# Kernel tuning notes

Hardware: AMD Instinct MI355X
Metric: run time of the kernel (lower is better)

## Reference

```python
import jax, jax.numpy as jnp
import numpy as np

N_HEADS = 16


def setup_inputs() -> dict:
    key = jax.random.key(0)
    ks = jax.random.split(key, 6)
    B, S, E = 2, 2048, 1024
    scale = 1.0 / np.sqrt(E)
    return {
        "X": jax.random.normal(ks[0], (B, S, E), dtype=jnp.float32),
        "Wq": jax.random.normal(ks[1], (E, E), dtype=jnp.float32) * scale,
        "Wk": jax.random.normal(ks[2], (E, E), dtype=jnp.float32) * scale,
        "Wv": jax.random.normal(ks[3], (E, E), dtype=jnp.float32) * scale,
        "Wp": jax.random.normal(ks[4], (E, E), dtype=jnp.float32) * scale,
        "bp": jnp.zeros((E,), dtype=jnp.float32),
    }


def reference(X, Wq, Wk, Wv, Wp, bp):
    B, S, E = X.shape
    H = N_HEADS
    dk = E // H
    # qkv projections (Linear with weight [out,in] -> x @ W.T), split heads
    q = (X @ Wq.T).reshape(B, S, H, dk).transpose(0, 2, 1, 3)  # [B,H,S,dk]
    k = (X @ Wk.T).reshape(B, S, H, dk).transpose(0, 2, 1, 3)
    v = (X @ Wv.T).reshape(B, S, H, dk).transpose(0, 2, 1, 3)
    scores = jnp.einsum('bhqd,bhkd->bhqk', q, k) / jnp.sqrt(jnp.asarray(dk, X.dtype))
    causal = jnp.tril(jnp.ones((S, S), dtype=bool))  # [S,S]
    scores = jnp.where(causal[None, None], scores, jnp.asarray(-jnp.inf, X.dtype))
    attn = jax.nn.softmax(scores, axis=-1)  # [B,H,S,S]
    y = jnp.einsum('bhqk,bhkd->bhqd', attn, v)  # [B,H,S,dk]
    y = y.transpose(0, 2, 1, 3).reshape(B, S, E)
    return y @ Wp.T + bp
```

## Files before the change

### kernel.cpp

```cpp
#include <hip/hip_runtime.h>

typedef unsigned short u16;
typedef __bf16 bf16x8 __attribute__((ext_vector_type(8)));
typedef float f32x4 __attribute__((ext_vector_type(4)));
typedef unsigned short u16x8 __attribute__((ext_vector_type(8)));
typedef unsigned short u16x4 __attribute__((ext_vector_type(4)));

union B8 { u16x8 u; bf16x8 b; };

#define MFMA_BF16(a, b, c) __builtin_amdgcn_mfma_f32_16x16x32_bf16((a), (b), (c), 0, 0, 0)

__device__ __forceinline__ u16 f2bf(float f) {
  unsigned x = __float_as_uint(f);
  unsigned r = x + 0x7fffu + ((x >> 16) & 1u);
  return (u16)(r >> 16);
}

__device__ __forceinline__ unsigned cvt_pk_bf16(float lo, float hi) {
  unsigned r;
  asm("v_cvt_pk_bf16_f32 %0, %1, %2" : "=v"(r) : "v"(lo), "v"(hi));
  return r;
}

__device__ __forceinline__ void gl2lds16(const void* g, void* l) {
  __builtin_amdgcn_global_load_lds(
      (const __attribute__((address_space(1))) void*)g,
      (__attribute__((address_space(3))) void*)l, 16, 0, 0);
}

__global__ __launch_bounds__(256) void cast5_kernel(
    const float* __restrict__ X, const float* __restrict__ Wq,
    const float* __restrict__ Wk, const float* __restrict__ Wv,
    const float* __restrict__ Wp, u16* __restrict__ Xb, u16* __restrict__ Wqb,
    u16* __restrict__ Wkb, u16* __restrict__ Wvb, u16* __restrict__ Wpb) {
  size_t i = ((size_t)blockIdx.x * 256 + threadIdx.x) * 4;
  const float* src;
  u16* dst;
  size_t off;
  if (i < 4194304) {
    src = X; dst = Xb; off = i;
  } else if (i < 5242880) {
    src = Wq; dst = Wqb; off = i - 4194304;
  } else if (i < 6291456) {
    src = Wk; dst = Wkb; off = i - 5242880;
  } else if (i < 7340032) {
    src = Wv; dst = Wvb; off = i - 6291456;
  } else {
    src = Wp; dst = Wpb; off = i - 7340032;
  }
  float4 v = *(const float4*)(src + off);
  u16x4 o;
  o[0] = f2bf(v.x); o[1] = f2bf(v.y); o[2] = f2bf(v.z); o[3] = f2bf(v.w);
  *(u16x4*)(dst + off) = o;
}

template <int N0>
__device__ __forceinline__ void mfma16(f32x4 (&acc)[8][4], B8 (&af)[8], B8& b0,
                                       B8& b1) {
  __builtin_amdgcn_s_setprio(1);
#pragma unroll
  for (int m = 0; m < 8; ++m) {
    acc[m][N0] = MFMA_BF16(af[m].b, b0.b, acc[m][N0]);
    acc[m][N0 + 1] = MFMA_BF16(af[m].b, b1.b, acc[m][N0 + 1]);
  }
  __builtin_amdgcn_s_setprio(0);
}

__global__ __launch_bounds__(512, 2) void gemm_qkv256(
    const u16* __restrict__ Xb, const u16* __restrict__ Wb,
    u16* __restrict__ Qb, u16* __restrict__ Kb, u16* __restrict__ Vt) {
  __shared__ __align__(16) u16 Al[2][2][256 * 32];
  __shared__ __align__(16) u16 Bl[2][2][256 * 32];

  int tid = threadIdx.x, lane = tid & 63, w = tid >> 6;
  int wr = w >> 2, wc = w & 3;
  int l16 = lane & 15, lg = lane >> 4;

  int bid = blockIdx.x;
  int swz = (bid & 7) * 24 + (bid >> 3);
  int bm = swz / 12, bn = swz % 12;

  const u16* Ag = Xb + (size_t)bm * 256 * 1024;
  const u16* Bg = Wb + (size_t)bn * 256 * 1024;

  int srow = w * 16 + (lane >> 2);
  int scol = lane & 3;

  auto stA = [&](int buf, int kh, int kt) {
#pragma unroll
    for (int p2 = 0; p2 < 2; ++p2) {
      int r = p2 * 128 + srow;
      int sl = scol ^ ((r >> 1) & 3);
      gl2lds16(Ag + (size_t)r * 1024 + kt * 64 + kh * 32 + sl * 8,
               (char*)&Al[buf][kh][0] + (size_t)(p2 * 128 + w * 16) * 64);
    }
  };
  auto stB = [&](int buf, int kh, int kt) {
#pragma unroll
    for (int p2 = 0; p2 < 2; ++p2) {
      int r = p2 * 128 + srow;
      int sl = scol ^ ((r >> 1) & 3);
      gl2lds16(Bg + (size_t)r * 1024 + kt * 64 + kh * 32 + sl * 8,
               (char*)&Bl[buf][kh][0] + (size_t)(p2 * 128 + w * 16) * 64);
    }
  };
  auto ldA = [&](int buf, int kk, B8 (&af)[8]) {
#pragma unroll
    for (int m = 0; m < 8; ++m) {
      int r = wr * 128 + m * 16 + l16;
      af[m].u = *(const u16x8*)((const char*)&Al[buf][kk][0] + r * 64 +
                                ((lg ^ ((r >> 1) & 3)) << 4));
    }
  };
  auto ldB = [&](int buf, int kk, int nf, B8& bf) {
    int r = wc * 64 + nf * 16 + l16;
    bf.u = *(const u16x8*)((const char*)&Bl[buf][kk][0] + r * 64 +
                           ((lg ^ ((r >> 1) & 3)) << 4));
  };

  f32x4 acc[8][4] = {};

  stA(0, 0, 0); stB(0, 0, 0);
  stA(0, 1, 0); stB(0, 1, 0);
  stA(1, 0, 1); stB(1, 0, 1);
  asm volatile("s_waitcnt vmcnt(8)" ::: "memory");
  __builtin_amdgcn_s_barrier();

  B8 af[8], b0, b1;
  for (int I = 0; I < 8; ++I) {
    int p = 2 * I;
    bool last = (I == 7);
    stA(1, 1, p + 1);
    ldA(0, 0, af); ldB(0, 0, 0, b0); ldB(0, 0, 1, b1);
    mfma16<0>(acc, af, b0, b1);
    stB(1, 1, p + 1);
    ldB(0, 0, 2, b0); ldB(0, 0, 3, b1);
    mfma16<2>(acc, af, b0, b1);
    if (last) asm volatile("s_waitcnt vmcnt(0)" ::: "memory");
    else      asm volatile("s_waitcnt vmcnt(8)" ::: "memory");
    __builtin_amdgcn_s_barrier();
    if (!last) stA(0, 0, p + 2);
    ldA(0, 1, af); ldB(0, 1, 0, b0); ldB(0, 1, 1, b1);
    mfma16<0>(acc, af, b0, b1);
    if (!last) stB(0, 0, p + 2);
    ldB(0, 1, 2, b0); ldB(0, 1, 3, b1);
    mfma16<2>(acc, af, b0, b1);
    if (last) asm volatile("s_waitcnt vmcnt(0)" ::: "memory");
    else      asm volatile("s_waitcnt vmcnt(8)" ::: "memory");
    __builtin_amdgcn_s_barrier();
    if (!last) stA(0, 1, p + 2);
    ldA(1, 0, af); ldB(1, 0, 0, b0); ldB(1, 0, 1, b1);
    mfma16<0>(acc, af, b0, b1);
    if (!last) stB(0, 1, p + 2);
    ldB(1, 0, 2, b0); ldB(1, 0, 3, b1);
    mfma16<2>(acc, af, b0, b1);
    if (last) asm volatile("s_waitcnt vmcnt(0)" ::: "memory");
    else      asm volatile("s_waitcnt vmcnt(8)" ::: "memory");
    __builtin_amdgcn_s_barrier();
    if (!last) stA(1, 0, p + 3);
    ldA(1, 1, af); ldB(1, 1, 0, b0); ldB(1, 1, 1, b1);
    mfma16<0>(acc, af, b0, b1);
    if (!last) stB(1, 0, p + 3);
    ldB(1, 1, 2, b0); ldB(1, 1, 3, b1);
    mfma16<2>(acc, af, b0, b1);
    if (!last) {
      asm volatile("s_waitcnt vmcnt(8)" ::: "memory");
      __builtin_amdgcn_s_barrier();
    }
  }

  const float QSCALE = 0.18033688011112042f;
#pragma unroll
  for (int m = 0; m < 8; ++m)
#pragma unroll
    for (int nf = 0; nf < 4; ++nf) {
      int colg = bn * 256 + wc * 64 + nf * 16 + l16;
      int rowg = bm * 256 + wr * 128 + m * 16 + lg * 4;
      if (bn < 4) {
#pragma unroll
        for (int j = 0; j < 4; ++j)
          Qb[(size_t)(rowg + j) * 1024 + colg] = f2bf(acc[m][nf][j] * QSCALE);
      } else if (bn < 8) {
#pragma unroll
        for (int j = 0; j < 4; ++j)
          Kb[(size_t)(rowg + j) * 1024 + (colg - 1024)] = f2bf(acc[m][nf][j]);
      } else {
        int cv = colg - 2048;
        int hh = cv >> 6, d = cv & 63;
        int bb = rowg >> 11, s0 = rowg & 2047;
        u16x4 pk;
#pragma unroll
        for (int j = 0; j < 4; ++j) pk[j] = f2bf(acc[m][nf][j]);
        *(u16x4*)(Vt + ((size_t)(bb * 16 + hh) * 64 + d) * 2048 + s0) = pk;
      }
    }
}

__device__ __forceinline__ void gemm_body(const u16* __restrict__ A,
                                          const u16* __restrict__ Bw,
                                          float* __restrict__ Cout,
                                          const float* __restrict__ bias,
                                          int bm, int bn, u16* Asm, u16* Bsm) {
  const int Kd = 1024, N = 1024;
  int tid = threadIdx.x;
  int lane = tid & 63, w = tid >> 6;
  int wr = w >> 1, wc = w & 1;
  int l16 = lane & 15, lg = lane >> 4;

  const u16* Abase = A + (size_t)bm * 128 * Kd;
  const u16* Bbase = Bw + (size_t)bn * 128 * Kd;

  f32x4 acc[4][4] = {};

  for (int kt = 0; kt < Kd / 64; ++kt) {
    int k0 = kt * 64;
#pragma unroll
    for (int i = 0; i < 4; ++i) {
      int uu = i * 256 + tid;
      int r = uu >> 3;
      int s = (uu & 7) ^ (r & 7);
      gl2lds16(Abase + (size_t)r * Kd + k0 + s * 8, Asm + i * 2048 + w * 512);
      gl2lds16(Bbase + (size_t)r * Kd + k0 + s * 8, Bsm + i * 2048 + w * 512);
    }
    asm volatile("s_waitcnt vmcnt(0)" ::: "memory");
    __syncthreads();

    B8 af[4][2], bfr[4][2];
#pragma unroll
    for (int mi = 0; mi < 4; ++mi)
#pragma unroll
      for (int kk = 0; kk < 2; ++kk) {
        int r = wr * 64 + mi * 16 + l16;
        int s = kk * 4 + lg;
        af[mi][kk].u = *(const u16x8*)((const char*)Asm + r * 128 + ((s ^ (r & 7)) << 4));
      }
#pragma unroll
    for (int ni = 0; ni < 4; ++ni)
#pragma unroll
      for (int kk = 0; kk < 2; ++kk) {
        int r = wc * 64 + ni * 16 + l16;
        int s = kk * 4 + lg;
        bfr[ni][kk].u = *(const u16x8*)((const char*)Bsm + r * 128 + ((s ^ (r & 7)) << 4));
      }
#pragma unroll
    for (int mi = 0; mi < 4; ++mi)
#pragma unroll
      for (int ni = 0; ni < 4; ++ni) {
        acc[mi][ni] = MFMA_BF16(af[mi][0].b, bfr[ni][0].b, acc[mi][ni]);
        acc[mi][ni] = MFMA_BF16(af[mi][1].b, bfr[ni][1].b, acc[mi][ni]);
      }
    __syncthreads();
  }

#pragma unroll
  for (int mi = 0; mi < 4; ++mi)
#pragma unroll
    for (int ni = 0; ni < 4; ++ni) {
      int col = bn * 128 + wc * 64 + ni * 16 + l16;
#pragma unroll
      for (int j = 0; j < 4; ++j) {
        int row = bm * 128 + wr * 64 + mi * 16 + lg * 4 + j;
        Cout[(size_t)row * N + col] = acc[mi][ni][j] + bias[col];
      }
    }
}

__global__ __launch_bounds__(256) void gemm_proj_kernel(
    const u16* __restrict__ Y1, const u16* __restrict__ Wpb,
    float* __restrict__ out, const float* __restrict__ bias) {
  __shared__ __align__(16) u16 Asm[128 * 64];
  __shared__ __align__(16) u16 Bsm[128 * 64];
  gemm_body(Y1, Wpb, out, bias, blockIdx.y, blockIdx.x, Asm, Bsm);
}

__global__ __launch_bounds__(256, 4) void attn_kernel(const u16* __restrict__ Q,
                                                      const u16* __restrict__ K,
                                                      const u16* __restrict__ Vt,
                                                      u16* __restrict__ Y) {
  __shared__ __align__(16) u16 Kl[2][64 * 64];
  __shared__ __align__(16) u16 Vl[2][64 * 64];
  __shared__ __align__(16) u16 Pl[4][16 * 64];

  const int E = 1024, S = 2048;
  int tid = threadIdx.x;
  int lane = tid & 63, w = tid >> 6;
  int l16 = lane & 15, lg = lane >> 4;
  int h7 = l16 & 7;

  int bid = blockIdx.x;
  int bh = bid & 31;
  int u = bid >> 5;
  int g = u & 7, kq = u >> 3;
  int qt = (kq == 0) ? 31 - g : (kq == 1) ? 16 + g : (kq == 2) ? 15 - g : g;
  int b = bh >> 4, h = bh & 15;

  const u16* Qb = Q + (size_t)b * S * E + (size_t)h * 64;
  const u16* Kb = K + (size_t)b * S * E + (size_t)h * 64;
  const u16* Vb = Vt + (size_t)bh * 64 * 2048;

  int r0 = tid >> 3;
  int s0 = (tid & 7) ^ (r0 & 7);
  size_t koff = (size_t)r0 * 1024 + s0 * 8;
  size_t voff = (size_t)r0 * 2048 + s0 * 8;
  const u16* kpA = Kb;
  const u16* kpB = Kb + 32 * 1024;
  const u16* vpA = Vb;
  const u16* vpB = Vb + 32 * 2048;

  const char* kbase0 = (const char*)&Kl[0][0] + l16 * 128 + ((lg ^ h7) << 4);
  const char* kbase1 = (const char*)&Kl[0][0] + l16 * 128 + (((4 + lg) ^ h7) << 4);
  const char* vbase0 = (const char*)&Vl[0][0] + l16 * 128 + ((lg ^ h7) << 4);
  const char* vbase1 = (const char*)&Vl[0][0] + l16 * 128 + (((4 + lg) ^ h7) << 4);
  char* pw0 = (char*)&Pl[w][0] + l16 * 128 + (((0 * 2 + (lg >> 1)) ^ h7) << 4) + (lg & 1) * 8;
  char* pw1 = (char*)&Pl[w][0] + l16 * 128 + (((1 * 2 + (lg >> 1)) ^ h7) << 4) + (lg & 1) * 8;
  char* pw2 = (char*)&Pl[w][0] + l16 * 128 + (((2 * 2 + (lg >> 1)) ^ h7) << 4) + (lg & 1) * 8;
  char* pw3 = (char*)&Pl[w][0] + l16 * 128 + (((3 * 2 + (lg >> 1)) ^ h7) << 4) + (lg & 1) * 8;
  const char* pr0 = (const char*)&Pl[w][0] + l16 * 128 + ((lg ^ h7) << 4);
  const char* pr1 = (const char*)&Pl[w][0] + l16 * 128 + (((4 + lg) ^ h7) << 4);

  B8 qa[2];
#pragma unroll
  for (int kk = 0; kk < 2; ++kk)
    qa[kk].u = *(const u16x8*)(Qb + (size_t)(qt * 64 + w * 16 + l16) * E + kk * 32 + lg * 8);

  f32x4 o[4] = {};
  float lrun = 0.f;
  int qrow = w * 16 + l16;

  gl2lds16(kpA + koff, &Kl[0][w * 512]);
  gl2lds16(vpA + voff, &Vl[0][w * 512]);
  gl2lds16(kpB + koff, &Kl[0][2048 + w * 512]);
  gl2lds16(vpB + voff, &Vl[0][2048 + w * 512]);
  kpA += 65536; kpB += 65536; vpA += 64; vpB += 64;

#define ATTN_ITER(BF, DOMASK, DOSTAGE)                                         \
  do {                                                                         \
    asm volatile("s_waitcnt vmcnt(0)" ::: "memory");                           \
    __syncthreads();                                                           \
    if (DOSTAGE) {                                                             \
      gl2lds16(kpA + koff, &Kl[(BF) ^ 1][w * 512]);                            \
      gl2lds16(vpA + voff, &Vl[(BF) ^ 1][w * 512]);                            \
      gl2lds16(kpB + koff, &Kl[(BF) ^ 1][2048 + w * 512]);                     \
      gl2lds16(vpB + voff, &Vl[(BF) ^ 1][2048 + w * 512]);                     \
      kpA += 65536; kpB += 65536; vpA += 64; vpB += 64;                        \
    }                                                                          \
    f32x4 sa[4] = {};                                                          \
    __builtin_amdgcn_s_setprio(1);                                             \
    _Pragma("unroll") for (int nb = 0; nb < 4; ++nb) {                         \
      B8 kf0, kf1;                                                             \
      kf0.u = *(const u16x8*)(kbase0 + (BF)*8192 + nb * 2048);                 \
      kf1.u = *(const u16x8*)(kbase1 + (BF)*8192 + nb * 2048);                 \
      sa[nb] = MFMA_BF16(kf0.b, qa[0].b, sa[nb]);                              \
      sa[nb] = MFMA_BF16(kf1.b, qa[1].b, sa[nb]);                              \
    }                                                                          \
    __builtin_amdgcn_s_setprio(0);                                             \
    float p[16];                                                               \
    _Pragma("unroll") for (int nb = 0; nb < 4; ++nb)                           \
        _Pragma("unroll") for (int j = 0; j < 4; ++j) {                        \
      float pe = __builtin_amdgcn_exp2f(sa[nb][j]);                            \
      if (DOMASK) {                                                            \
        int kv = nb * 16 + lg * 4 + j;                                         \
        if (kv > qrow) pe = 0.f;                                               \
      }                                                                        \
      p[nb * 4 + j] = pe;                                                      \
    }                                                                          \
    {                                                                          \
      union { u16x4 v; unsigned uu[2]; } pk;                                   \
      pk.uu[0] = cvt_pk_bf16(p[0], p[1]);                                      \
      pk.uu[1] = cvt_pk_bf16(p[2], p[3]);                                      \
      *(u16x4*)pw0 = pk.v;                                                     \
      pk.uu[0] = cvt_pk_bf16(p[4], p[5]);                                      \
      pk.uu[1] = cvt_pk_bf16(p[6], p[7]);                                      \
      *(u16x4*)pw1 = pk.v;                                                     \
      pk.uu[0] = cvt_pk_bf16(p[8], p[9]);                                      \
      pk.uu[1] = cvt_pk_bf16(p[10], p[11]);                                    \
      *(u16x4*)pw2 = pk.v;                                                     \
      pk.uu[0] = cvt_pk_bf16(p[12], p[13]);                                    \
      pk.uu[1] = cvt_pk_bf16(p[14], p[15]);                                    \
      *(u16x4*)pw3 = pk.v;                                                     \
    }                                                                          \
    lrun += ((p[0] + p[1]) + (p[2] + p[3])) + ((p[4] + p[5]) + (p[6] + p[7])) +\
            ((p[8] + p[9]) + (p[10] + p[11])) +                                \
            ((p[12] + p[13]) + (p[14] + p[15]));                               \
    B8 pa0, pa1;                                                               \
    pa0.u = *(const u16x8*)pr0;                                                \
    pa1.u = *(const u16x8*)pr1;                                                \
    __builtin_amdgcn_s_setprio(1);                                             \
    _Pragma("unroll") for (int nb = 0; nb < 4; ++nb) {                         \
      B8 vf0, vf1;                                                             \
      vf0.u = *(const u16x8*)(vbase0 + (BF)*8192 + nb * 2048);                 \
      vf1.u = *(const u16x8*)(vbase1 + (BF)*8192 + nb * 2048);                 \
      o[nb] = MFMA_BF16(pa0.b, vf0.b, o[nb]);                                  \
      o[nb] = MFMA_BF16(pa1.b, vf1.b, o[nb]);                                  \
    }                                                                          \
    __builtin_amdgcn_s_setprio(0);                                             \
  } while (0)

  int U = qt;
  int i = 0;
  for (; i + 2 <= U; i += 2) {
    ATTN_ITER(0, false, true);
    ATTN_ITER(1, false, true);
  }
  if (U & 1) {
    ATTN_ITER(0, false, true);
    ATTN_ITER(1, true, false);
  } else {
    ATTN_ITER(0, true, false);
  }
#undef ATTN_ITER

  lrun += __shfl_xor(lrun, 16);
  lrun += __shfl_xor(lrun, 32);
  float inv[4];
#pragma unroll
  for (int j = 0; j < 4; ++j) {
    float lj = __shfl(lrun, (lane & 48) | (lg * 4 + j));
    inv[j] = 1.0f / lj;
  }
#pragma unroll
  for (int nb = 0; nb < 4; ++nb)
#pragma unroll
    for (int j = 0; j < 4; ++j) {
      int row = qt * 64 + w * 16 + lg * 4 + j;
      int col = h * 64 + nb * 16 + l16;
      Y[((size_t)b * S + row) * E + col] = f2bf(o[nb][j] * inv[j]);
    }
}

extern "C" void kernel_launch(void* const* d_in, const int* in_sizes, int n_in,
                              void* d_out, int out_size, void* d_ws,
                              size_t ws_size, hipStream_t stream) {
  const float* X = (const float*)d_in[0];
  const float* Wq = (const float*)d_in[1];
  const float* Wk = (const float*)d_in[2];
  const float* Wv = (const float*)d_in[3];
  const float* Wp = (const float*)d_in[4];
  const float* bp = (const float*)d_in[5];
  float* out = (float*)d_out;

  char* ws = (char*)d_ws;
  const size_t MB = 1ull << 20;
  u16* Xb = (u16*)(ws + 0 * MB);
  u16* Wqb = (u16*)(ws + 8 * MB);
  u16* Wkb = (u16*)(ws + 10 * MB);
  u16* Wvb = (u16*)(ws + 12 * MB);
  u16* Wpb = (u16*)(ws + 14 * MB);
  u16* Qb = (u16*)(ws + 16 * MB);
  u16* Kb = (u16*)(ws + 24 * MB);
  u16* VtB = (u16*)(ws + 32 * MB);
  u16* Y1 = (u16*)(ws + 40 * MB);

  cast5_kernel<<<8192, 256, 0, stream>>>(X, Wq, Wk, Wv, Wp, Xb, Wqb, Wkb, Wvb, Wpb);
  gemm_qkv256<<<192, 512, 0, stream>>>(Xb, Wqb, Qb, Kb, VtB);
  attn_kernel<<<1024, 256, 0, stream>>>(Qb, Kb, VtB, Y1);
  gemm_proj_kernel<<<dim3(8, 32), 256, 0, stream>>>(Y1, Wpb, out, bp);
}
```

Measured before the change: 104.1 us.

## Double-buffer projection GEMM and load V fragments directly from global in attention

The output projection GEMM now uses two LDS buffers, prefetching the next K-tile while the current one is computed. This removes the trailing barrier, and MFMAs get raised priority. In attention, V is no longer staged through LDS: each wave loads its V fragments straight from global memory into registers every iteration. The block-to-(batch,head) mapping is also permuted. The aim is to cut LDS traffic and barrier stalls, at the risk of exposing global-load latency for V on the critical path.

```diff
diff --git a/kernel.cpp b/kernel.cpp
--- a/kernel.cpp
+++ b/kernel.cpp
@@ -196,34 +196,44 @@
     }
 }
 
-__device__ __forceinline__ void gemm_body(const u16* __restrict__ A,
-                                          const u16* __restrict__ Bw,
-                                          float* __restrict__ Cout,
-                                          const float* __restrict__ bias,
-                                          int bm, int bn, u16* Asm, u16* Bsm) {
+__global__ __launch_bounds__(256) void gemm_proj_kernel(
+    const u16* __restrict__ Y1, const u16* __restrict__ Wpb,
+    float* __restrict__ out, const float* __restrict__ bias) {
+  __shared__ __align__(16) u16 Asm[2][128 * 64];
+  __shared__ __align__(16) u16 Bsm[2][128 * 64];
+
   const int Kd = 1024, N = 1024;
+  int bm = blockIdx.y, bn = blockIdx.x;
   int tid = threadIdx.x;
   int lane = tid & 63, w = tid >> 6;
   int wr = w >> 1, wc = w & 1;
   int l16 = lane & 15, lg = lane >> 4;
 
-  const u16* Abase = A + (size_t)bm * 128 * Kd;
-  const u16* Bbase = Bw + (size_t)bn * 128 * Kd;
+  const u16* Abase = Y1 + (size_t)bm * 128 * Kd;
+  const u16* Bbase = Wpb + (size_t)bn * 128 * Kd;
+
+  int r0 = tid >> 3;
+
+  auto stage = [&](int buf, int kt) {
+#pragma unroll
+    for (int i = 0; i < 4; ++i) {
+      int r = i * 32 + r0;
+      int sl = (tid & 7) ^ (r & 7);
+      gl2lds16(Abase + (size_t)r * Kd + kt * 64 + sl * 8,
+               &Asm[buf][i * 2048 + w * 512]);
+      gl2lds16(Bbase + (size_t)r * Kd + kt * 64 + sl * 8,
+               &Bsm[buf][i * 2048 + w * 512]);
+    }
+  };
 
   f32x4 acc[4][4] = {};
-
-  for (int kt = 0; kt < Kd / 64; ++kt) {
-    int k0 = kt * 64;
-#pragma unroll
-    for (int i = 0; i < 4; ++i) {
-      int uu = i * 256 + tid;
-      int r = uu >> 3;
-      int s = (uu & 7) ^ (r & 7);
-      gl2lds16(Abase + (size_t)r * Kd + k0 + s * 8, Asm + i * 2048 + w * 512);
-      gl2lds16(Bbase + (size_t)r * Kd + k0 + s * 8, Bsm + i * 2048 + w * 512);
-    }
+  stage(0, 0);
+  int buf = 0;
+
+  for (int kt = 0; kt < 16; ++kt) {
     asm volatile("s_waitcnt vmcnt(0)" ::: "memory");
     __syncthreads();
+    if (kt + 1 < 16) stage(buf ^ 1, kt + 1);
 
     B8 af[4][2], bfr[4][2];
 #pragma unroll
@@ -232,7 +242,8 @@
       for (int kk = 0; kk < 2; ++kk) {
         int r = wr * 64 + mi * 16 + l16;
         int s = kk * 4 + lg;
-        af[mi][kk].u = *(const u16x8*)((const char*)Asm + r * 128 + ((s ^ (r & 7)) << 4));
+        af[mi][kk].u = *(const u16x8*)((const char*)&Asm[buf][0] + r * 128 +
+                                       ((s ^ (r & 7)) << 4));
       }
 #pragma unroll
     for (int ni = 0; ni < 4; ++ni)
@@ -240,8 +251,10 @@
       for (int kk = 0; kk < 2; ++kk) {
         int r = wc * 64 + ni * 16 + l16;
         int s = kk * 4 + lg;
-        bfr[ni][kk].u = *(const u16x8*)((const char*)Bsm + r * 128 + ((s ^ (r & 7)) << 4));
+        bfr[ni][kk].u = *(const u16x8*)((const char*)&Bsm[buf][0] + r * 128 +
+                                        ((s ^ (r & 7)) << 4));
       }
+    __builtin_amdgcn_s_setprio(1);
 #pragma unroll
     for (int mi = 0; mi < 4; ++mi)
 #pragma unroll
@@ -249,7 +262,8 @@
         acc[mi][ni] = MFMA_BF16(af[mi][0].b, bfr[ni][0].b, acc[mi][ni]);
         acc[mi][ni] = MFMA_BF16(af[mi][1].b, bfr[ni][1].b, acc[mi][ni]);
       }
-    __syncthreads();
+    __builtin_amdgcn_s_setprio(0);
+    buf ^= 1;
   }
 
 #pragma unroll
@@ -260,17 +274,9 @@
 #pragma unroll
       for (int j = 0; j < 4; ++j) {
         int row = bm * 128 + wr * 64 + mi * 16 + lg * 4 + j;
-        Cout[(size_t)row * N + col] = acc[mi][ni][j] + bias[col];
+        out[(size_t)row * N + col] = acc[mi][ni][j] + bias[col];
       }
     }
-}
-
-__global__ __launch_bounds__(256) void gemm_proj_kernel(
-    const u16* __restrict__ Y1, const u16* __restrict__ Wpb,
-    float* __restrict__ out, const float* __restrict__ bias) {
-  __shared__ __align__(16) u16 Asm[128 * 64];
-  __shared__ __align__(16) u16 Bsm[128 * 64];
-  gemm_body(Y1, Wpb, out, bias, blockIdx.y, blockIdx.x, Asm, Bsm);
 }
 
 __global__ __launch_bounds__(256, 4) void attn_kernel(const u16* __restrict__ Q,
@@ -278,7 +284,6 @@
                                                       const u16* __restrict__ Vt,
                                                       u16* __restrict__ Y) {
   __shared__ __align__(16) u16 Kl[2][64 * 64];
-  __shared__ __align__(16) u16 Vl[2][64 * 64];
   __shared__ __align__(16) u16 Pl[4][16 * 64];
 
   const int E = 1024, S = 2048;
@@ -288,7 +293,7 @@
   int h7 = l16 & 7;
 
   int bid = blockIdx.x;
-  int bh = bid & 31;
+  int bh = (bid & 7) * 4 + ((bid >> 3) & 3);
   int u = bid >> 5;
   int g = u & 7, kq = u >> 3;
   int qt = (kq == 0) ? 31 - g : (kq == 1) ? 16 + g : (kq == 2) ? 15 - g : g;
@@ -301,16 +306,16 @@
   int r0 = tid >> 3;
   int s0 = (tid & 7) ^ (r0 & 7);
   size_t koff = (size_t)r0 * 1024 + s0 * 8;
-  size_t voff = (size_t)r0 * 2048 + s0 * 8;
   const u16* kpA = Kb;
   const u16* kpB = Kb + 32 * 1024;
-  const u16* vpA = Vb;
-  const u16* vpB = Vb + 32 * 2048;
+
+  const u16* vg0 = Vb + (size_t)(0 * 16 + l16) * 2048 + lg * 8;
+  const u16* vg1 = Vb + (size_t)(1 * 16 + l16) * 2048 + lg * 8;
+  const u16* vg2 = Vb + (size_t)(2 * 16 + l16) * 2048 + lg * 8;
+  const u16* vg3 = Vb + (size_t)(3 * 16 + l16) * 2048 + lg * 8;
 
   const char* kbase0 = (const char*)&Kl[0][0] + l16 * 128 + ((lg ^ h7) << 4);
   const char* kbase1 = (const char*)&Kl[0][0] + l16 * 128 + (((4 + lg) ^ h7) << 4);
-  const char* vbase0 = (const char*)&Vl[0][0] + l16 * 128 + ((lg ^ h7) << 4);
-  const char* vbase1 = (const char*)&Vl[0][0] + l16 * 128 + (((4 + lg) ^ h7) << 4);
   char* pw0 = (char*)&Pl[w][0] + l16 * 128 + (((0 * 2 + (lg >> 1)) ^ h7) << 4) + (lg & 1) * 8;
   char* pw1 = (char*)&Pl[w][0] + l16 * 128 + (((1 * 2 + (lg >> 1)) ^ h7) << 4) + (lg & 1) * 8;
   char* pw2 = (char*)&Pl[w][0] + l16 * 128 + (((2 * 2 + (lg >> 1)) ^ h7) << 4) + (lg & 1) * 8;
@@ -328,10 +333,8 @@
   int qrow = w * 16 + l16;
 
   gl2lds16(kpA + koff, &Kl[0][w * 512]);
-  gl2lds16(vpA + voff, &Vl[0][w * 512]);
   gl2lds16(kpB + koff, &Kl[0][2048 + w * 512]);
-  gl2lds16(vpB + voff, &Vl[0][2048 + w * 512]);
-  kpA += 65536; kpB += 65536; vpA += 64; vpB += 64;
+  kpA += 65536; kpB += 65536;
 
 #define ATTN_ITER(BF, DOMASK, DOSTAGE)                                         \
   do {                                                                         \
@@ -339,10 +342,8 @@
     __syncthreads();                                                           \
     if (DOSTAGE) {                                                             \
       gl2lds16(kpA + koff, &Kl[(BF) ^ 1][w * 512]);                            \
-      gl2lds16(vpA + voff, &Vl[(BF) ^ 1][w * 512]);                            \
       gl2lds16(kpB + koff, &Kl[(BF) ^ 1][2048 + w * 512]);                     \
-      gl2lds16(vpB + voff, &Vl[(BF) ^ 1][2048 + w * 512]);                     \
-      kpA += 65536; kpB += 65536; vpA += 64; vpB += 64;                        \
+      kpA += 65536; kpB += 65536;                                              \
     }                                                                          \
     f32x4 sa[4] = {};                                                          \
     __builtin_amdgcn_s_setprio(1);                                             \
@@ -354,6 +355,16 @@
       sa[nb] = MFMA_BF16(kf1.b, qa[1].b, sa[nb]);                              \
     }                                                                          \
     __builtin_amdgcn_s_setprio(0);                                             \
+    B8 vf[4][2];                                                               \
+    vf[0][0].u = *(const u16x8*)(vg0);                                         \
+    vf[0][1].u = *(const u16x8*)(vg0 + 32);                                    \
+    vf[1][0].u = *(const u16x8*)(vg1);                                         \
+    vf[1][1].u = *(const u16x8*)(vg1 + 32);                                    \
+    vf[2][0].u = *(const u16x8*)(vg2);                                         \
+    vf[2][1].u = *(const u16x8*)(vg2 + 32);                                    \
+    vf[3][0].u = *(const u16x8*)(vg3);                                         \
+    vf[3][1].u = *(const u16x8*)(vg3 + 32);                                    \
+    vg0 += 64; vg1 += 64; vg2 += 64; vg3 += 64;                                \
     float p[16];                                                               \
     _Pragma("unroll") for (int nb = 0; nb < 4; ++nb)                           \
         _Pragma("unroll") for (int j = 0; j < 4; ++j) {                        \
@@ -387,11 +398,8 @@
     pa1.u = *(const u16x8*)pr1;                                                \
     __builtin_amdgcn_s_setprio(1);                                             \
     _Pragma("unroll") for (int nb = 0; nb < 4; ++nb) {                         \
-      B8 vf0, vf1;                                                             \
-      vf0.u = *(const u16x8*)(vbase0 + (BF)*8192 + nb * 2048);                 \
-      vf1.u = *(const u16x8*)(vbase1 + (BF)*8192 + nb * 2048);                 \
-      o[nb] = MFMA_BF16(pa0.b, vf0.b, o[nb]);                                  \
-      o[nb] = MFMA_BF16(pa1.b, vf1.b, o[nb]);                                  \
+      o[nb] = MFMA_BF16(pa0.b, vf[nb][0].b, o[nb]);                            \
+      o[nb] = MFMA_BF16(pa1.b, vf[nb][1].b, o[nb]);                            \
     }                                                                          \
     __builtin_amdgcn_s_setprio(0);                                             \
   } while (0)
```

Result: slower. 151.2 us (+45.3%).
